# Kernel tuning notes

Measured on AMD Instinct MI355X. Metric: run time of the kernel, lower is better.

## Reference

```python
import jax, jax.numpy as jnp
import numpy as np

EPS_ATTN = 1e-5   # attention denominator eps (module eps)
EPS_LN = 1e-5     # nn.LayerNorm default eps


def _prime(x, proj):
    # Performer FAVOR+ hyperbolic positive features.
    # x: (B,H,L,dh), proj: (dh,m) -> (B,H,L,2m)
    dn = x.shape[-1] ** -0.25
    xn = dn * x
    d = jnp.einsum('bhld,dm->bhlm', xn, proj)
    diag = 0.5 * jnp.sum(xn * xn, axis=-1, keepdims=True)
    return jnp.concatenate([jnp.exp(d - diag), jnp.exp(-d - diag)], axis=-1)


def setup_inputs() -> dict:
    L, B, H, DH, DM, M = 2048, 4, 8, 64, 512, 256
    key = jax.random.key(0)
    k0, k1, k2 = jax.random.split(key, 3)
    h = jax.random.normal(k0, (L, B, DM), jnp.float32)
    w_qkv = jax.random.normal(k1, (H * 3 * DH, DM), jnp.float32) / np.sqrt(DM)
    w_o = jax.random.normal(k2, (DM, H * DH), jnp.float32) / np.sqrt(H * DH)
    ln_gamma = jnp.ones((DM,), jnp.float32)
    ln_beta = jnp.zeros((DM,), jnp.float32)
    # Gaussian orthogonal random matrix (blockwise QR), rows scaled by sqrt(dh)
    rng = np.random.default_rng(0)
    blocks = []
    for _ in range(M // DH):
        g = rng.standard_normal((DH, DH)).astype(np.float32)
        q, _ = np.linalg.qr(g)
        blocks.append(q.T)
    pm = np.concatenate(blocks, axis=0) * np.sqrt(DH)  # (M, DH)
    proj_matrix = jnp.asarray(pm.T.astype(np.float32))  # (DH, M)
    return {"h": h, "w_qkv": w_qkv, "w_o": w_o,
            "ln_gamma": ln_gamma, "ln_beta": ln_beta,
            "proj_matrix": proj_matrix}


def _forward(h, w_qkv, w_o, ln_gamma, ln_beta, proj_matrix):
    L, B, DM = h.shape
    DH, M = proj_matrix.shape
    H = w_qkv.shape[0] // (3 * DH)
    scale = DH ** -0.5

    qkv = (h @ w_qkv.T).reshape(L, B, H, 3 * DH)
    q, k, v = jnp.split(qkv, 3, axis=-1)
    q = jnp.transpose(q, (1, 2, 0, 3))  # (B,H,L,dh)
    k = jnp.transpose(k, (1, 2, 0, 3))
    v = jnp.transpose(v, (1, 2, 0, 3))

    qp = _prime(q, proj_matrix)  # (B,H,L,2M)
    kp = _prime(k, proj_matrix)
    kp = kp / jnp.sum(kp, axis=-1, keepdims=True)
    qp = qp / jnp.sum(qp, axis=-1, keepdims=True)

    den_acc = jnp.cumsum(kp, axis=2)
    denom = jnp.einsum('bhlm,bhlm->bhl', den_acc, qp)[..., None]  # (B,H,L,1)

    # fast_weight_sum: W_t = W_{t-1} + k_t v_t^T ; out_t = q_t @ W_t
    def step(W, xs):
        qt, kt, vt = xs  # (B,H,2M), (B,H,2M), (B,H,dh)
        W = W + kt[..., :, None] * vt[..., None, :]
        out = jnp.einsum('bhm,bhmd->bhd', qt, W)
        return W, out

    W0 = jnp.zeros((B, H, 2 * M, DH), h.dtype)
    xs = (jnp.transpose(qp, (2, 0, 1, 3)),
          jnp.transpose(kp, (2, 0, 1, 3)),
          jnp.transpose(v, (2, 0, 1, 3)))
    _, out = jax.lax.scan(step, W0, xs)  # (L,B,H,dh)
    out = jnp.transpose(out, (1, 2, 0, 3))  # (B,H,L,dh)

    out = scale * out / (denom + EPS_ATTN)
    out = jnp.transpose(out, (0, 2, 1, 3)).reshape(B, L, H * DH)  # (B,L,H*dh)
    out = jnp.swapaxes(out, 0, 1)  # (L,B,H*dh)

    attn_out = out @ w_o.T
    x = h + attn_out
    mu = jnp.mean(x, axis=-1, keepdims=True)
    var = jnp.mean((x - mu) ** 2, axis=-1, keepdims=True)
    return (x - mu) / jnp.sqrt(var + EPS_LN) * ln_gamma + ln_beta


def reference(h, w_qkv, w_o, ln_gamma, ln_beta, proj_matrix):
    return _forward(h, w_qkv, w_o, ln_gamma, ln_beta, proj_matrix)
```

## Files before the change

### kernel.cpp

```cpp
#include <hip/hip_runtime.h>
#include <hip/hip_fp16.h>
#include <math.h>

#define LSEQ 2048
#define NB 4
#define NH 8
#define DMID 512
#define CHK 128
#define SCALE 0.125f
#define DN 0.35355339059327373f
#define DN2 0.125f
#define LOG2E 1.4426950408889634f
#define EPS_ATTN 1e-5f
#define EPS_LN 1e-5f

typedef _Float16 f16x8 __attribute__((ext_vector_type(8)));
typedef _Float16 f16x4 __attribute__((ext_vector_type(4)));
typedef float f32x4 __attribute__((ext_vector_type(4)));

__device__ __forceinline__ float exp2a(float x) {
  float r;
  asm("v_exp_f32 %0, %1" : "=v"(r) : "v"(x));
  return r;
}

__device__ __forceinline__ void cvt16(const float* __restrict__ p,
                                      _Float16* __restrict__ dst) {
  float4 a = *(const float4*)p, b = *(const float4*)(p + 4);
  float4 c = *(const float4*)(p + 8), d = *(const float4*)(p + 12);
  f16x8 t0 = {(_Float16)a.x, (_Float16)a.y, (_Float16)a.z, (_Float16)a.w,
              (_Float16)b.x, (_Float16)b.y, (_Float16)b.z, (_Float16)b.w};
  f16x8 t1 = {(_Float16)c.x, (_Float16)c.y, (_Float16)c.z, (_Float16)c.w,
              (_Float16)d.x, (_Float16)d.y, (_Float16)d.z, (_Float16)d.w};
  *(f16x8*)dst = t0;
  *(f16x8*)(dst + 8) = t1;
}

__global__ void k_diag(float* out, int n, float val) {
  int i = blockIdx.x * 256 + threadIdx.x;
  if (i < n) out[i] = val;
}

__global__ __launch_bounds__(256) void k_ptr(const float* __restrict__ proj,
                                             __half* __restrict__ projT) {
  int e = blockIdx.x * 256 + threadIdx.x;
  int n = e >> 6, k = e & 63;
  projT[e] = __float2half_rn(proj[k * 256 + n] * (DN * LOG2E));
}

__global__ __launch_bounds__(256) void k_qkv(
    const float* __restrict__ A, const float* __restrict__ Wq,
    __half* __restrict__ q, __half* __restrict__ k, __half* __restrict__ v) {
  __shared__ __align__(16) char smem[34816];
  _Float16* Ah = (_Float16*)smem;
  _Float16* Bh = (_Float16*)(smem + 10240);
  _Float16* Oh = (_Float16*)smem;

  const int tid = threadIdx.x;
  const int row0 = blockIdx.x * 128;
  const int col0 = blockIdx.y * 128;
  const int lane = tid & 63, wv = tid >> 6;
  const int ln15 = lane & 15, quad = lane >> 4;
  const int m0 = wv * 32;
  const int srow = tid >> 1, sc = (tid & 1) * 16;

  f32x4 Cacc[2][8];
  const f32x4 z4 = {0.f, 0.f, 0.f, 0.f};
#pragma unroll
  for (int mi = 0; mi < 2; ++mi)
#pragma unroll
    for (int nt = 0; nt < 8; ++nt) Cacc[mi][nt] = z4;

  for (int kt = 0; kt < DMID; kt += 32) {
    cvt16(A + (size_t)(row0 + srow) * DMID + kt + sc, &Ah[srow * 40 + sc]);
    cvt16(Wq + (size_t)(col0 + srow) * DMID + kt + sc, &Bh[srow * 40 + sc]);
    __syncthreads();
    f16x8 a0 = *(const f16x8*)&Ah[(m0 + ln15) * 40 + quad * 8];
    f16x8 a1 = *(const f16x8*)&Ah[(m0 + 16 + ln15) * 40 + quad * 8];
#pragma unroll
    for (int nt = 0; nt < 8; ++nt) {
      f16x8 bf = *(const f16x8*)&Bh[(nt * 16 + ln15) * 40 + quad * 8];
      Cacc[0][nt] = __builtin_amdgcn_mfma_f32_16x16x32_f16(a0, bf, Cacc[0][nt], 0, 0, 0);
      Cacc[1][nt] = __builtin_amdgcn_mfma_f32_16x16x32_f16(a1, bf, Cacc[1][nt], 0, 0, 0);
    }
    __syncthreads();
  }
#pragma unroll
  for (int mi = 0; mi < 2; ++mi)
#pragma unroll
    for (int nt = 0; nt < 8; ++nt)
#pragma unroll
      for (int r = 0; r < 4; ++r)
        Oh[(m0 + mi * 16 + quad * 4 + r) * 136 + nt * 16 + ln15] =
            (_Float16)Cacc[mi][nt][r];
  __syncthreads();
  const int tr = tid >> 4, tc = tid & 15;
  const int col = col0 + tc * 8;
  const int hh = col / 192;
  const int rem = col - hh * 192;
  const int t = rem >> 6;
  const int d0 = rem & 63;
  __half* dstb = (t == 0) ? q : ((t == 1) ? k : v);
#pragma unroll
  for (int i = 0; i < 8; ++i) {
    int lrow = tr * 8 + i;
    int grow = row0 + lrow;
    int l = grow >> 2, bb = grow & 3;
    f16x8 val = *(const f16x8*)&Oh[lrow * 136 + tc * 8];
    *(f16x8*)((_Float16*)dstb + (((size_t)(bb * NH + hh) * LSEQ + l) << 6) + d0) = val;
  }
}

__global__ __launch_bounds__(512) void k_dgemm(
    const __half* __restrict__ qsrc, const __half* __restrict__ ksrc,
    const __half* __restrict__ projT, __half* __restrict__ dqd,
    __half* __restrict__ dkd, float* __restrict__ nq,
    float* __restrict__ nk) {
  __shared__ __align__(16) char smem[37888];
  _Float16* Bt = (_Float16*)smem;
  float* g_l  = (float*)(smem + 36864);
  float* ps_l = (float*)(smem + 37376);
  _Float16* Oh = (_Float16*)smem;

  const int tid = threadIdx.x;
  const __half* src = blockIdx.y ? ksrc : qsrc;
  __half* dst = blockIdx.y ? dkd : dqd;
  float* nrm = blockIdx.y ? nk : nq;
  const size_t r0 = (size_t)blockIdx.x * 128;

  const int lane = tid & 63, wv = tid >> 6;
  const int ln15 = lane & 15, quad = lane >> 4;
  const int m0 = wv * 16;

#pragma unroll
  for (int it = 0; it < 4; ++it) {
    int e = it * 512 + tid;
    int n = e >> 3, seg = e & 7;
    *(f16x8*)&Bt[n * 72 + seg * 8] =
        *(const f16x8*)((const _Float16*)projT + n * 64 + seg * 8);
  }

  f16x8 afrag[2];
  float ss = 0.f;
  {
    const _Float16* rp = (const _Float16*)src + (r0 + m0 + ln15) * 64;
#pragma unroll
    for (int ks = 0; ks < 2; ++ks) {
      f16x8 x8 = *(const f16x8*)(rp + ks * 32 + quad * 8);
      afrag[ks] = x8;
#pragma unroll
      for (int j = 0; j < 8; ++j) {
        float xv = (float)x8[j];
        ss = fmaf(xv, xv, ss);
      }
    }
    ss += __shfl_xor(ss, 16);
    ss += __shfl_xor(ss, 32);
  }
  if (quad == 0) g_l[m0 + ln15] = 0.5f * DN2 * LOG2E * ss;
  __syncthreads();

  f32x4 Cacc[16];
  const f32x4 z4 = {0.f, 0.f, 0.f, 0.f};
#pragma unroll
  for (int nt = 0; nt < 16; ++nt) Cacc[nt] = z4;

#pragma unroll
  for (int ks = 0; ks < 2; ++ks) {
    f16x8 a0 = afrag[ks];
#pragma unroll
    for (int nt = 0; nt < 16; ++nt) {
      f16x8 bf = *(const f16x8*)&Bt[(nt * 16 + ln15) * 72 + ks * 32 + quad * 8];
      Cacc[nt] = __builtin_amdgcn_mfma_f32_16x16x32_f16(a0, bf, Cacc[nt], 0, 0, 0);
    }
  }

  float gv[4], pp[4];
#pragma unroll
  for (int r = 0; r < 4; ++r) {
    gv[r] = g_l[m0 + quad * 4 + r];
    pp[r] = 0.f;
  }
#pragma unroll
  for (int nt = 0; nt < 16; ++nt)
#pragma unroll
    for (int r = 0; r < 4; ++r) {
      float d = Cacc[nt][r];
      pp[r] += exp2a(d - gv[r]) + exp2a(-d - gv[r]);
    }
#pragma unroll
  for (int r = 0; r < 4; ++r) {
    float p = pp[r];
    p += __shfl_xor(p, 1); p += __shfl_xor(p, 2);
    p += __shfl_xor(p, 4); p += __shfl_xor(p, 8);
    if (ln15 == 0) ps_l[m0 + quad * 4 + r] = p;
  }

#pragma unroll
  for (int hf = 0; hf < 2; ++hf) {
    __syncthreads();
#pragma unroll
    for (int nt2 = 0; nt2 < 8; ++nt2) {
      int nt = hf * 8 + nt2;
#pragma unroll
      for (int r = 0; r < 4; ++r)
        Oh[(m0 + quad * 4 + r) * 136 + nt2 * 16 + ln15] =
            (_Float16)Cacc[nt][r];
    }
    __syncthreads();
#pragma unroll
    for (int it = 0; it < 4; ++it) {
      int e = it * 512 + tid;
      int row = e >> 4, seg = e & 15;
      *(f16x8*)((_Float16*)dst + (r0 + row) * 256 + hf * 128 + seg * 8) =
          *(const f16x8*)&Oh[row * 136 + seg * 8];
    }
  }
  if (tid < 128) nrm[r0 + tid] = g_l[tid] + __log2f(ps_l[tid]);
}

__global__ __launch_bounds__(256) void k_kv(
    const __half* __restrict__ dk, const float* __restrict__ nk,
    const __half* __restrict__ v, __half* __restrict__ KVt,
    float* __restrict__ Ks) {
  __shared__ __align__(16) char smem[53248];
  _Float16* kpT = (_Float16*)smem;
  _Float16* Vt  = (_Float16*)(smem + 34816);
  float* ck = (float*)(smem + 52224);
  _Float16* Oh2 = (_Float16*)smem;

  const int tid = threadIdx.x;
  const int cidx = blockIdx.x;
  const int i0 = blockIdx.y * 128;
  const float fsign = (i0 < 256) ? 1.f : -1.f;
  const int m0col = (i0 < 256) ? i0 : i0 - 256;
  const size_t rowbase = (size_t)cidx * CHK;

  if (tid < 128) ck[tid] = nk[rowbase + tid];
  __syncthreads();

  {
    const int srow = tid >> 1;
    const int scol = (tid & 1) * 64;
    float c = ck[srow];
    const _Float16* src =
        (const _Float16*)dk + (rowbase + srow) * 256 + m0col + scol;
#pragma unroll
    for (int it = 0; it < 8; ++it) {
      f16x8 d8 = *(const f16x8*)(src + it * 8);
#pragma unroll
      for (int j = 0; j < 8; ++j)
        kpT[(scol + it * 8 + j) * 136 + srow] =
            (_Float16)exp2a(fmaf((float)d8[j], fsign, -c));
    }
  }
  {
    int s = tid & 127, dq0 = (tid >> 7) * 32;
    const _Float16* vsrc = (const _Float16*)v + (rowbase + s) * 64 + dq0;
#pragma unroll
    for (int b8 = 0; b8 < 4; ++b8) {
      f16x8 v8 = ((const f16x8*)vsrc)[b8];
#pragma unroll
      for (int j = 0; j < 8; ++j)
        Vt[(dq0 + b8 * 8 + j) * 136 + s] = v8[j];
    }
  }
  __syncthreads();

  const int lane = tid & 63, wv = tid >> 6;
  const int ln15 = lane & 15, quad = lane >> 4;
  const int m0 = wv * 32;

  f32x4 Cacc[2][4], Kacc[2];
  const f32x4 z4 = {0.f, 0.f, 0.f, 0.f};
#pragma unroll
  for (int mi = 0; mi < 2; ++mi) {
#pragma unroll
    for (int nt = 0; nt < 4; ++nt) Cacc[mi][nt] = z4;
    Kacc[mi] = z4;
  }
  f16x8 bone;
#pragma unroll
  for (int j = 0; j < 8; ++j)
    bone[j] = (ln15 == 0) ? (_Float16)1.0f : (_Float16)0.0f;

#pragma unroll
  for (int ks = 0; ks < 4; ++ks) {
    f16x8 a0 = *(const f16x8*)&kpT[(m0 + ln15) * 136 + ks * 32 + quad * 8];
    f16x8 a1 = *(const f16x8*)&kpT[(m0 + 16 + ln15) * 136 + ks * 32 + quad * 8];
#pragma unroll
    for (int nt = 0; nt < 4; ++nt) {
      f16x8 bV = *(const f16x8*)&Vt[(nt * 16 + ln15) * 136 + ks * 32 + quad * 8];
      Cacc[0][nt] = __builtin_amdgcn_mfma_f32_16x16x32_f16(a0, bV, Cacc[0][nt], 0, 0, 0);
      Cacc[1][nt] = __builtin_amdgcn_mfma_f32_16x16x32_f16(a1, bV, Cacc[1][nt], 0, 0, 0);
    }
    Kacc[0] = __builtin_amdgcn_mfma_f32_16x16x32_f16(a0, bone, Kacc[0], 0, 0, 0);
    Kacc[1] = __builtin_amdgcn_mfma_f32_16x16x32_f16(a1, bone, Kacc[1], 0, 0, 0);
  }

  if (ln15 == 0) {
#pragma unroll
    for (int mi = 0; mi < 2; ++mi)
#pragma unroll
      for (int r = 0; r < 4; ++r)
        Ks[(size_t)cidx * 512 + i0 + m0 + mi * 16 + quad * 4 + r] = Kacc[mi][r];
  }
  __syncthreads();
#pragma unroll
  for (int mi = 0; mi < 2; ++mi)
#pragma unroll
    for (int nt = 0; nt < 4; ++nt) {
      f16x4 pack = {(_Float16)Cacc[mi][nt][0], (_Float16)Cacc[mi][nt][1],
                    (_Float16)Cacc[mi][nt][2], (_Float16)Cacc[mi][nt][3]};
      *(f16x4*)&Oh2[(nt * 16 + ln15) * 136 + m0 + mi * 16 + quad * 4] = pack;
    }
  __syncthreads();
  {
    int d = tid >> 2, part = tid & 3;
    _Float16* dstp =
        (_Float16*)KVt + (size_t)cidx * 32768 + d * 512 + i0 + part * 32;
    const _Float16* srcp = &Oh2[d * 136 + part * 32];
#pragma unroll
    for (int j = 0; j < 4; ++j)
      *(f16x8*)(dstp + j * 8) = *(const f16x8*)(srcp + j * 8);
  }
}

__global__ __launch_bounds__(256) void k_scan(__half2* __restrict__ KV2,
                                              float* __restrict__ Ks) {
  const int bh = blockIdx.x;
  const int tid = threadIdx.x;
  if (blockIdx.y < 32) {
    uint2* p = (uint2*)(KV2 + (size_t)bh * 262144) + (blockIdx.y * 256 + tid);
    uint2 raw[16];
#pragma unroll
    for (int c = 0; c < 16; ++c) raw[c] = p[c * 8192];
    float ax0 = 0.f, ay0 = 0.f, ax1 = 0.f, ay1 = 0.f;
#pragma unroll
    for (int c = 0; c < 16; ++c) {
      __half2 h0 = *(__half2*)&raw[c].x;
      __half2 h1 = *(__half2*)&raw[c].y;
      float2 f0 = __half22float2(h0), f1 = __half22float2(h1);
      __half2 o0 = __floats2half2_rn(ax0, ay0);
      __half2 o1 = __floats2half2_rn(ax1, ay1);
      uint2 o;
      o.x = *(unsigned*)&o0;
      o.y = *(unsigned*)&o1;
      p[c * 8192] = o;
      ax0 += f0.x; ay0 += f0.y; ax1 += f1.x; ay1 += f1.y;
    }
  } else {
    int i = (blockIdx.y - 32) * 256 + tid;
    float* pk = Ks + (size_t)bh * 8192 + i;
    float vs[16];
#pragma unroll
    for (int c = 0; c < 16; ++c) vs[c] = pk[c * 512];
    float a = 0.f;
#pragma unroll
    for (int c = 0; c < 16; ++c) { pk[c * 512] = a; a += vs[c]; }
  }
}

template <int TH>
__device__ __forceinline__ void attn_body(
    const __half* __restrict__ dq, const __half* __restrict__ dk,
    const float* __restrict__ nq, const float* __restrict__ nk,
    const __half* __restrict__ v, const __half* __restrict__ KVt,
    const float* __restrict__ Kpre, float* __restrict__ outb, int cidx,
    char* smem) {
  constexpr int KROWS = TH ? 128 : 64;
  constexpr int KR32 = KROWS / 32;
  constexpr int NS = TH ? 8 : 4;
  constexpr int NKS = TH ? 4 : 2;

  _Float16* qpT = (_Float16*)(smem);
  _Float16* kpT = (_Float16*)(smem + 9216);
  _Float16* WT  = (_Float16*)(smem + 27648);
  float*    KpT = (float*)(smem + 36864);
  _Float16* S_h = (_Float16*)(smem);
  _Float16* Vt  = (_Float16*)(smem + 17408);
  float* cq_l   = (float*)(smem + 37120);
  float* ck_l   = (float*)(smem + 37632);
  float* den1_l = (float*)(smem + 38656);
  float* den2_l = (float*)(smem + 38912);
  float* invd_l = (float*)(smem + 39168);

  const int tid = threadIdx.x;
  const int cc = cidx & 15, bh = cidx >> 4;
  const size_t rowb = (size_t)cidx * 128;
  const size_t rowt = rowb + TH * 64;
  const int lane = tid & 63;
  const int wv = tid >> 6;
  const int ln15 = lane & 15;
  const int quad = lane >> 4;
  const int m0 = wv * 16;

  if (tid < 64) cq_l[tid] = nq[rowt + tid];
  if (tid < KROWS) ck_l[tid] = nk[rowb + tid];
  __syncthreads();

  const int c8 = tid & 7;
  const int r8 = tid >> 3;
  const int csrc = (c8 & 3) * 8;
  const float sgnf = (c8 < 4) ? 1.f : -1.f;

  const _Float16* qsrc = (const _Float16*)dq + (rowt + r8) * 256 + csrc;
  const _Float16* ksrc = (const _Float16*)dk + (rowb + r8) * 256 + csrc;
  const _Float16* wsrc = (const _Float16*)KVt + (size_t)cidx * 32768 +
                         r8 * 512 + ((c8 < 4) ? 0 : 256) + csrc;
  const float* kpsrc = Kpre + (size_t)cidx * 512 +
                       ((tid < 32) ? tid : (tid < 64 ? 224 + tid : 0));

  float cq[2], ck[KR32];
#pragma unroll
  for (int p = 0; p < 2; ++p) cq[p] = cq_l[r8 + p * 32];
#pragma unroll
  for (int p = 0; p < KR32; ++p) ck[p] = ck_l[r8 + p * 32];

  f16x8 rq[2], rk[KR32];
#pragma unroll
  for (int p = 0; p < 2; ++p) rq[p] = *(const f16x8*)(qsrc + p * 8192);
#pragma unroll
  for (int p = 0; p < KR32; ++p) rk[p] = *(const f16x8*)(ksrc + p * 8192);

  f32x4 Sacc[NS], Oacc[4], Dacc;
  const f32x4 z4 = {0.f, 0.f, 0.f, 0.f};
#pragma unroll
  for (int nt = 0; nt < NS; ++nt) Sacc[nt] = z4;
#pragma unroll
  for (int nt = 0; nt < 4; ++nt) Oacc[nt] = z4;
  Dacc = z4;

  for (int it = 0; it < 8; ++it) {
    const int kb = it * 32;
    f16x8 w0 = *(const f16x8*)(wsrc + kb);
    f16x8 w1 = *(const f16x8*)(wsrc + 16384 + kb);
    float kp = kpsrc[kb];

#pragma unroll
    for (int p = 0; p < 2; ++p) {
      f16x8 d = rq[p], t;
#pragma unroll
      for (int j = 0; j < 8; ++j)
        t[j] = (_Float16)exp2a(fmaf((float)d[j], sgnf, -cq[p]));
      *(f16x8*)&qpT[(r8 + p * 32) * 72 + c8 * 8] = t;
    }
#pragma unroll
    for (int p = 0; p < KR32; ++p) {
      f16x8 d = rk[p], t;
#pragma unroll
      for (int j = 0; j < 8; ++j)
        t[j] = (_Float16)exp2a(fmaf((float)d[j], sgnf, -ck[p]));
      *(f16x8*)&kpT[(r8 + p * 32) * 72 + c8 * 8] = t;
    }

    if (it < 7) {
#pragma unroll
      for (int p = 0; p < 2; ++p)
        rq[p] = *(const f16x8*)(qsrc + p * 8192 + kb + 32);
#pragma unroll
      for (int p = 0; p < KR32; ++p)
        rk[p] = *(const f16x8*)(ksrc + p * 8192 + kb + 32);
    }
    *(f16x8*)&WT[r8 * 72 + c8 * 8] = w0;
    *(f16x8*)&WT[(r8 + 32) * 72 + c8 * 8] = w1;
    if (tid < 64) KpT[tid] = kp;

    asm volatile("s_waitcnt lgkmcnt(0)" ::: "memory");
    __builtin_amdgcn_s_barrier();
    asm volatile("" ::: "memory");

#pragma unroll
    for (int ks = 0; ks < 2; ++ks) {
      f16x8 a0 = *(const f16x8*)&qpT[(m0 + ln15) * 72 + ks * 32 + quad * 8];
#pragma unroll
      for (int nt = 0; nt < NS; ++nt) {
        f16x8 bf = *(const f16x8*)&kpT[(nt * 16 + ln15) * 72 + ks * 32 + quad * 8];
        Sacc[nt] = __builtin_amdgcn_mfma_f32_16x16x32_f16(a0, bf, Sacc[nt], 0, 0, 0);
      }
#pragma unroll
      for (int nt = 0; nt < 4; ++nt) {
        f16x8 bw = *(const f16x8*)&WT[(nt * 16 + ln15) * 72 + ks * 32 + quad * 8];
        Oacc[nt] = __builtin_amdgcn_mfma_f32_16x16x32_f16(a0, bw, Oacc[nt], 0, 0, 0);
      }
      f16x8 bk;
#pragma unroll
      for (int j = 0; j < 8; ++j)
        bk[j] = (ln15 == 0) ? (_Float16)KpT[ks * 32 + quad * 8 + j]
                            : (_Float16)0.f;
      Dacc = __builtin_amdgcn_mfma_f32_16x16x32_f16(a0, bk, Dacc, 0, 0, 0);
    }

    asm volatile("" ::: "memory");
    __builtin_amdgcn_s_barrier();
    asm volatile("" ::: "memory");
  }

  if (ln15 == 0) {
#pragma unroll
    for (int r = 0; r < 4; ++r)
      den2_l[m0 + quad * 4 + r] = Dacc[r];
  }
  {
    float dp[4] = {0.f, 0.f, 0.f, 0.f};
#pragma unroll
    for (int nt = 0; nt < NS; ++nt) {
      int s = nt * 16 + ln15;
#pragma unroll
      for (int r = 0; r < 4; ++r) {
        int tl = m0 + quad * 4 + r;
        float vsv = (s <= TH * 64 + tl) ? Sacc[nt][r] : 0.f;
        dp[r] += vsv;
        S_h[tl * 136 + s] = (_Float16)vsv;
      }
    }
#pragma unroll
    for (int r = 0; r < 4; ++r) {
      float p = dp[r];
      p += __shfl_xor(p, 1); p += __shfl_xor(p, 2);
      p += __shfl_xor(p, 4); p += __shfl_xor(p, 8);
      if (ln15 == 0) den1_l[m0 + quad * 4 + r] = p;
    }
  }
  __syncthreads();
  if (tid < 64)
    invd_l[tid] = SCALE / (den1_l[tid] + den2_l[tid] + EPS_ATTN);
  {
    int s = tid & 127, d0v = (tid >> 7) * 32;
    if (TH == 1 || s < 64) {
      const _Float16* vsrc = (const _Float16*)v + (rowb + s) * 64 + d0v;
      f16x8 v0 = ((const f16x8*)vsrc)[0];
      f16x8 v1 = ((const f16x8*)vsrc)[1];
      f16x8 v2 = ((const f16x8*)vsrc)[2];
      f16x8 v3 = ((const f16x8*)vsrc)[3];
#pragma unroll
      for (int j = 0; j < 8; ++j) {
        Vt[(d0v + j) * 136 + s] = v0[j];
        Vt[(d0v + 8 + j) * 136 + s] = v1[j];
        Vt[(d0v + 16 + j) * 136 + s] = v2[j];
        Vt[(d0v + 24 + j) * 136 + s] = v3[j];
      }
    }
  }
  __syncthreads();
#pragma unroll
  for (int ks = 0; ks < NKS; ++ks) {
    f16x8 aS0 = *(const f16x8*)&S_h[(m0 + ln15) * 136 + ks * 32 + quad * 8];
#pragma unroll
    for (int nt = 0; nt < 4; ++nt) {
      f16x8 bV = *(const f16x8*)&Vt[(nt * 16 + ln15) * 136 + ks * 32 + quad * 8];
      Oacc[nt] = __builtin_amdgcn_mfma_f32_16x16x32_f16(aS0, bV, Oacc[nt], 0, 0, 0);
    }
  }
  const int b = bh >> 3, hh = bh & 7;
  float ivv[4];
#pragma unroll
  for (int r = 0; r < 4; ++r)
    ivv[r] = invd_l[m0 + quad * 4 + r];
#pragma unroll
  for (int nt = 0; nt < 4; ++nt) {
    int dcol = nt * 16 + ln15;
#pragma unroll
    for (int r = 0; r < 4; ++r) {
      int tl = m0 + quad * 4 + r;
      int l = cc * 128 + TH * 64 + tl;
      outb[((size_t)l * 4 + b) * 512 + hh * 64 + dcol] = Oacc[nt][r] * ivv[r];
    }
  }
}

__global__ __launch_bounds__(256, 4) void k_attn(
    const __half* __restrict__ dq, const __half* __restrict__ dk,
    const float* __restrict__ nq, const float* __restrict__ nk,
    const __half* __restrict__ v, const __half* __restrict__ KVt,
    const float* __restrict__ Kpre, float* __restrict__ outb) {
  __shared__ __align__(16) char smem[39424];
  const int bid = blockIdx.x;
  const int cidx = ((bid >> 4) << 3) + (bid & 7);
  if (((bid >> 3) & 1) == 0)
    attn_body<0>(dq, dk, nq, nk, v, KVt, Kpre, outb, cidx, smem);
  else
    attn_body<1>(dq, dk, nq, nk, v, KVt, Kpre, outb, cidx, smem);
}

__global__ __launch_bounds__(256) void k_oproj(
    const float* __restrict__ A, const float* __restrict__ Wo,
    const float* __restrict__ hres, float* __restrict__ xout) {
  __shared__ __align__(16) char smem[34816];
  _Float16* Ah = (_Float16*)smem;
  _Float16* Bh = (_Float16*)(smem + 10240);
  _Float16* Oh = (_Float16*)smem;

  const int tid = threadIdx.x;
  const int row0 = blockIdx.x * 128;
  const int col0 = blockIdx.y * 128;
  const int lane = tid & 63, wv = tid >> 6;
  const int ln15 = lane & 15, quad = lane >> 4;
  const int m0 = wv * 32;
  const int srow = tid >> 1, sc = (tid & 1) * 16;

  f32x4 Cacc[2][8];
  const f32x4 z4 = {0.f, 0.f, 0.f, 0.f};
#pragma unroll
  for (int mi = 0; mi < 2; ++mi)
#pragma unroll
    for (int nt = 0; nt < 8; ++nt) Cacc[mi][nt] = z4;

  for (int kt = 0; kt < DMID; kt += 32) {
    cvt16(A + (size_t)(row0 + srow) * DMID + kt + sc, &Ah[srow * 40 + sc]);
    cvt16(Wo + (size_t)(col0 + srow) * DMID + kt + sc, &Bh[srow * 40 + sc]);
    __syncthreads();
    f16x8 a0 = *(const f16x8*)&Ah[(m0 + ln15) * 40 + quad * 8];
    f16x8 a1 = *(const f16x8*)&Ah[(m0 + 16 + ln15) * 40 + quad * 8];
#pragma unroll
    for (int nt = 0; nt < 8; ++nt) {
      f16x8 bf = *(const f16x8*)&Bh[(nt * 16 + ln15) * 40 + quad * 8];
      Cacc[0][nt] = __builtin_amdgcn_mfma_f32_16x16x32_f16(a0, bf, Cacc[0][nt], 0, 0, 0);
      Cacc[1][nt] = __builtin_amdgcn_mfma_f32_16x16x32_f16(a1, bf, Cacc[1][nt], 0, 0, 0);
    }
    __syncthreads();
  }
#pragma unroll
  for (int mi = 0; mi < 2; ++mi)
#pragma unroll
    for (int nt = 0; nt < 8; ++nt)
#pragma unroll
      for (int r = 0; r < 4; ++r)
        Oh[(m0 + mi * 16 + quad * 4 + r) * 136 + nt * 16 + ln15] =
            (_Float16)Cacc[mi][nt][r];
  __syncthreads();
  const int tr = tid >> 4, tc = tid & 15;
#pragma unroll
  for (int i = 0; i < 8; ++i) {
    int lrow = tr * 8 + i;
    int grow = row0 + lrow;
    size_t base = (size_t)grow * 512 + col0 + tc * 8;
    f16x8 o = *(const f16x8*)&Oh[lrow * 136 + tc * 8];
    float4 h0 = *(const float4*)(hres + base);
    float4 h1 = *(const float4*)(hres + base + 4);
    *(float4*)(xout + base) =
        make_float4((float)o[0] + h0.x, (float)o[1] + h0.y,
                    (float)o[2] + h0.z, (float)o[3] + h0.w);
    *(float4*)(xout + base + 4) =
        make_float4((float)o[4] + h1.x, (float)o[5] + h1.y,
                    (float)o[6] + h1.z, (float)o[7] + h1.w);
  }
}

__global__ __launch_bounds__(256) void k_ln(float* __restrict__ x,
                                            const float* __restrict__ g,
                                            const float* __restrict__ bta) {
  __shared__ float ws_[4], wq_[4];
  const int row = blockIdx.x;
  const int tid = threadIdx.x;
  float2 vv = *(const float2*)(x + (size_t)row * 512 + tid * 2);
  float s = vv.x + vv.y;
  float sq = vv.x * vv.x + vv.y * vv.y;
#pragma unroll
  for (int off = 1; off < 64; off <<= 1) {
    s += __shfl_xor(s, off, 64);
    sq += __shfl_xor(sq, off, 64);
  }
  if ((tid & 63) == 0) { ws_[tid >> 6] = s; wq_[tid >> 6] = sq; }
  __syncthreads();
  s = ws_[0] + ws_[1] + ws_[2] + ws_[3];
  sq = wq_[0] + wq_[1] + wq_[2] + wq_[3];
  float mu = s * (1.f / 512.f);
  float var = sq * (1.f / 512.f) - mu * mu;
  float rstd = rsqrtf(var + EPS_LN);
  int c = tid * 2;
  float2 o;
  o.x = (vv.x - mu) * rstd * g[c] + bta[c];
  o.y = (vv.y - mu) * rstd * g[c + 1] + bta[c + 1];
  *(float2*)(x + (size_t)row * 512 + c) = o;
}

extern "C" void kernel_launch(void* const* d_in, const int* in_sizes, int n_in,
                              void* d_out, int out_size, void* d_ws,
                              size_t ws_size, hipStream_t stream) {
  const float* h    = (const float*)d_in[0];
  const float* wqkv = (const float*)d_in[1];
  const float* wo   = (const float*)d_in[2];
  const float* g    = (const float*)d_in[3];
  const float* bta  = (const float*)d_in[4];
  const float* proj = (const float*)d_in[5];
  float* out = (float*)d_out;
  char* wsb = (char*)d_ws;

  __half* q   = (__half*)(wsb + 0);
  __half* kb  = (__half*)(wsb + 8388608);
  __half* vb  = (__half*)(wsb + 16777216);
  __half* dq  = (__half*)(wsb + 25165824);
  __half* dk  = (__half*)(wsb + 58720256);
  float*  nq  = (float*)(wsb + 92274688);
  float*  nk  = (float*)(wsb + 92798976);
  __half* KVt = (__half*)(wsb + 93323264);
  float*  Ks  = (float*)(wsb + 126877696);
  __half* pT  = (__half*)(wsb + 127926272);
  float* outb = (float*)(wsb + 0);

  if (ws_size < 127959040ull) {
    float val = 1000.0f + (float)(ws_size >> 20);
    k_diag<<<(out_size + 255) / 256, 256, 0, stream>>>(out, out_size, val);
    return;
  }

  k_ptr  <<<dim3(64), 256, 0, stream>>>(proj, pT);
  k_qkv  <<<dim3(64, 12), 256, 0, stream>>>(h, wqkv, q, kb, vb);
  k_dgemm<<<dim3(512, 2), 512, 0, stream>>>(q, kb, pT, dq, dk, nq, nk);
  k_kv   <<<dim3(512, 4), 256, 0, stream>>>(dk, nk, vb, KVt, Ks);
  k_scan <<<dim3(32, 34), 256, 0, stream>>>((__half2*)KVt, Ks);
  k_attn <<<dim3(1024), 256, 0, stream>>>(dq, dk, nq, nk, vb, KVt, Ks, outb);
  k_oproj<<<dim3(64, 4), 256, 0, stream>>>(outb, wo, h, out);
  k_ln   <<<dim3(8192), 256, 0, stream>>>(out, g, bta);
}
```

Baseline: 246.2 us.

## Merge attention half-chunk blocks into one 512-thread block per chunk

Before, each 128-row chunk was handled by two 256-thread blocks, one per 64-row half, and each block recomputed the key features and reloaded the KV-state tile. Now a single 512-thread block processes the whole chunk: the key features, W tile and V transpose are computed once and shared by both halves, with the two half-groups of waves selected by a runtime flag. This removes duplicated exp work and global loads. In exchange, shared memory per block grows, the grid is halved, the two halves have unequal work inside one block, and the launch-bounds occupancy hint is dropped.

```diff
diff --git a/kernel.cpp b/kernel.cpp
--- a/kernel.cpp
+++ b/kernel.cpp
@@ -361,80 +361,77 @@
   }
 }
 
-template <int TH>
-__device__ __forceinline__ void attn_body(
+__global__ __launch_bounds__(512) void k_attn(
     const __half* __restrict__ dq, const __half* __restrict__ dk,
     const float* __restrict__ nq, const float* __restrict__ nk,
     const __half* __restrict__ v, const __half* __restrict__ KVt,
-    const float* __restrict__ Kpre, float* __restrict__ outb, int cidx,
-    char* smem) {
-  constexpr int KROWS = TH ? 128 : 64;
-  constexpr int KR32 = KROWS / 32;
-  constexpr int NS = TH ? 8 : 4;
-  constexpr int NKS = TH ? 4 : 2;
-
+    const float* __restrict__ Kpre, float* __restrict__ outb) {
+  __shared__ __align__(16) char smem[53760];
   _Float16* qpT = (_Float16*)(smem);
-  _Float16* kpT = (_Float16*)(smem + 9216);
-  _Float16* WT  = (_Float16*)(smem + 27648);
-  float*    KpT = (float*)(smem + 36864);
+  _Float16* kpT = (_Float16*)(smem + 18432);
+  _Float16* WT  = (_Float16*)(smem + 36864);
+  float*    KpT = (float*)(smem + 46080);
+  float* cq_l   = (float*)(smem + 46336);
+  float* ck_l   = (float*)(smem + 46848);
   _Float16* S_h = (_Float16*)(smem);
-  _Float16* Vt  = (_Float16*)(smem + 17408);
-  float* cq_l   = (float*)(smem + 37120);
-  float* ck_l   = (float*)(smem + 37632);
-  float* den1_l = (float*)(smem + 38656);
-  float* den2_l = (float*)(smem + 38912);
-  float* invd_l = (float*)(smem + 39168);
+  _Float16* Vt  = (_Float16*)(smem + 34816);
+  float* den1_l = (float*)(smem + 52224);
+  float* den2_l = (float*)(smem + 52736);
+  float* invd_l = (float*)(smem + 53248);
 
   const int tid = threadIdx.x;
+  const int cidx = blockIdx.x;
   const int cc = cidx & 15, bh = cidx >> 4;
   const size_t rowb = (size_t)cidx * 128;
-  const size_t rowt = rowb + TH * 64;
   const int lane = tid & 63;
   const int wv = tid >> 6;
-  const int ln15 = lane & 15;
-  const int quad = lane >> 4;
-  const int m0 = wv * 16;
-
-  if (tid < 64) cq_l[tid] = nq[rowt + tid];
-  if (tid < KROWS) ck_l[tid] = nk[rowb + tid];
+  const int H = wv >> 2;
+  const int m0 = (wv & 3) * 16;
+  const int ln15 = lane & 15, quad = lane >> 4;
+
+  if (tid < 128) cq_l[tid] = nq[rowb + tid];
+  else if (tid < 256) ck_l[tid - 128] = nk[rowb + tid - 128];
   __syncthreads();
 
   const int c8 = tid & 7;
-  const int r8 = tid >> 3;
+  const int r9 = tid >> 3;
   const int csrc = (c8 & 3) * 8;
   const float sgnf = (c8 < 4) ? 1.f : -1.f;
 
-  const _Float16* qsrc = (const _Float16*)dq + (rowt + r8) * 256 + csrc;
-  const _Float16* ksrc = (const _Float16*)dk + (rowb + r8) * 256 + csrc;
+  const _Float16* qsrc = (const _Float16*)dq + (rowb + r9) * 256 + csrc;
+  const _Float16* ksrc = (const _Float16*)dk + (rowb + r9) * 256 + csrc;
   const _Float16* wsrc = (const _Float16*)KVt + (size_t)cidx * 32768 +
-                         r8 * 512 + ((c8 < 4) ? 0 : 256) + csrc;
+                         r9 * 512 + ((c8 < 4) ? 0 : 256) + csrc;
   const float* kpsrc = Kpre + (size_t)cidx * 512 +
                        ((tid < 32) ? tid : (tid < 64 ? 224 + tid : 0));
 
-  float cq[2], ck[KR32];
-#pragma unroll
-  for (int p = 0; p < 2; ++p) cq[p] = cq_l[r8 + p * 32];
-#pragma unroll
-  for (int p = 0; p < KR32; ++p) ck[p] = ck_l[r8 + p * 32];
-
-  f16x8 rq[2], rk[KR32];
-#pragma unroll
-  for (int p = 0; p < 2; ++p) rq[p] = *(const f16x8*)(qsrc + p * 8192);
-#pragma unroll
-  for (int p = 0; p < KR32; ++p) rk[p] = *(const f16x8*)(ksrc + p * 8192);
-
-  f32x4 Sacc[NS], Oacc[4], Dacc;
+  float cq[2], ck2[2];
+#pragma unroll
+  for (int p = 0; p < 2; ++p) {
+    cq[p] = cq_l[r9 + p * 64];
+    ck2[p] = ck_l[r9 + p * 64];
+  }
+
+  f16x8 rq[2], rk[2];
+#pragma unroll
+  for (int p = 0; p < 2; ++p) {
+    rq[p] = *(const f16x8*)(qsrc + p * 16384);
+    rk[p] = *(const f16x8*)(ksrc + p * 16384);
+  }
+
+  f32x4 Sacc[8], Oacc[4], Dacc;
   const f32x4 z4 = {0.f, 0.f, 0.f, 0.f};
 #pragma unroll
-  for (int nt = 0; nt < NS; ++nt) Sacc[nt] = z4;
+  for (int nt = 0; nt < 8; ++nt) Sacc[nt] = z4;
 #pragma unroll
   for (int nt = 0; nt < 4; ++nt) Oacc[nt] = z4;
   Dacc = z4;
+
+  const int NSw = H ? 8 : 4;
 
   for (int it = 0; it < 8; ++it) {
     const int kb = it * 32;
     f16x8 w0 = *(const f16x8*)(wsrc + kb);
-    f16x8 w1 = *(const f16x8*)(wsrc + 16384 + kb);
     float kp = kpsrc[kb];
 
 #pragma unroll
@@ -443,27 +440,25 @@
 #pragma unroll
       for (int j = 0; j < 8; ++j)
         t[j] = (_Float16)exp2a(fmaf((float)d[j], sgnf, -cq[p]));
-      *(f16x8*)&qpT[(r8 + p * 32) * 72 + c8 * 8] = t;
-    }
-#pragma unroll
-    for (int p = 0; p < KR32; ++p) {
+      *(f16x8*)&qpT[(r9 + p * 64) * 72 + c8 * 8] = t;
+    }
+#pragma unroll
+    for (int p = 0; p < 2; ++p) {
       f16x8 d = rk[p], t;
 #pragma unroll
       for (int j = 0; j < 8; ++j)
-        t[j] = (_Float16)exp2a(fmaf((float)d[j], sgnf, -ck[p]));
-      *(f16x8*)&kpT[(r8 + p * 32) * 72 + c8 * 8] = t;
+        t[j] = (_Float16)exp2a(fmaf((float)d[j], sgnf, -ck2[p]));
+      *(f16x8*)&kpT[(r9 + p * 64) * 72 + c8 * 8] = t;
     }
 
     if (it < 7) {
 #pragma unroll
-      for (int p = 0; p < 2; ++p)
-        rq[p] = *(const f16x8*)(qsrc + p * 8192 + kb + 32);
-#pragma unroll
-      for (int p = 0; p < KR32; ++p)
-        rk[p] = *(const f16x8*)(ksrc + p * 8192 + kb + 32);
-    }
-    *(f16x8*)&WT[r8 * 72 + c8 * 8] = w0;
-    *(f16x8*)&WT[(r8 + 32) * 72 + c8 * 8] = w1;
+      for (int p = 0; p < 2; ++p) {
+        rq[p] = *(const f16x8*)(qsrc + p * 16384 + kb + 32);
+        rk[p] = *(const f16x8*)(ksrc + p * 16384 + kb + 32);
+      }
+    }
+    *(f16x8*)&WT[r9 * 72 + c8 * 8] = w0;
     if (tid < 64) KpT[tid] = kp;
 
     asm volatile("s_waitcnt lgkmcnt(0)" ::: "memory");
@@ -472,11 +467,18 @@
 
 #pragma unroll
     for (int ks = 0; ks < 2; ++ks) {
-      f16x8 a0 = *(const f16x8*)&qpT[(m0 + ln15) * 72 + ks * 32 + quad * 8];
-#pragma unroll
-      for (int nt = 0; nt < NS; ++nt) {
+      f16x8 a0 = *(const f16x8*)&qpT[(H * 64 + m0 + ln15) * 72 + ks * 32 + quad * 8];
+#pragma unroll
+      for (int nt = 0; nt < 4; ++nt) {
         f16x8 bf = *(const f16x8*)&kpT[(nt * 16 + ln15) * 72 + ks * 32 + quad * 8];
         Sacc[nt] = __builtin_amdgcn_mfma_f32_16x16x32_f16(a0, bf, Sacc[nt], 0, 0, 0);
+      }
+      if (H) {
+#pragma unroll
+        for (int nt = 4; nt < 8; ++nt) {
+          f16x8 bf = *(const f16x8*)&kpT[(nt * 16 + ln15) * 72 + ks * 32 + quad * 8];
+          Sacc[nt] = __builtin_amdgcn_mfma_f32_16x16x32_f16(a0, bf, Sacc[nt], 0, 0, 0);
+        }
       }
 #pragma unroll
       for (int nt = 0; nt < 4; ++nt) {
@@ -499,19 +501,22 @@
   if (ln15 == 0) {
 #pragma unroll
     for (int r = 0; r < 4; ++r)
-      den2_l[m0 + quad * 4 + r] = Dacc[r];
+      den2_l[H * 64 + m0 + quad * 4 + r] = Dacc[r];
   }
   {
+    _Float16* S_me = S_h + H * 8704;
     float dp[4] = {0.f, 0.f, 0.f, 0.f};
 #pragma unroll
-    for (int nt = 0; nt < NS; ++nt) {
-      int s = nt * 16 + ln15;
-#pragma unroll
-      for (int r = 0; r < 4; ++r) {
-        int tl = m0 + quad * 4 + r;
-        float vsv = (s <= TH * 64 + tl) ? Sacc[nt][r] : 0.f;
-        dp[r] += vsv;
-        S_h[tl * 136 + s] = (_Float16)vsv;
+    for (int nt = 0; nt < 8; ++nt) {
+      if (nt < NSw) {
+        int s = nt * 16 + ln15;
+#pragma unroll
+        for (int r = 0; r < 4; ++r) {
+          int tl = m0 + quad * 4 + r;
+          float vsv = (s <= H * 64 + tl) ? Sacc[nt][r] : 0.f;
+          dp[r] += vsv;
+          S_me[tl * 136 + s] = (_Float16)vsv;
+        }
       }
     }
 #pragma unroll
@@ -519,68 +524,52 @@
       float p = dp[r];
       p += __shfl_xor(p, 1); p += __shfl_xor(p, 2);
       p += __shfl_xor(p, 4); p += __shfl_xor(p, 8);
-      if (ln15 == 0) den1_l[m0 + quad * 4 + r] = p;
-    }
-  }
-  __syncthreads();
-  if (tid < 64)
+      if (ln15 == 0) den1_l[H * 64 + m0 + quad * 4 + r] = p;
+    }
+  }
+  {
+    int s = tid & 127, d0v = (tid >> 7) * 16;
+    const _Float16* vsrc = (const _Float16*)v + (rowb + s) * 64 + d0v;
+    f16x8 v0 = ((const f16x8*)vsrc)[0];
+    f16x8 v1 = ((const f16x8*)vsrc)[1];
+#pragma unroll
+    for (int j = 0; j < 8; ++j) {
+      Vt[(d0v + j) * 136 + s] = v0[j];
+      Vt[(d0v + 8 + j) * 136 + s] = v1[j];
+    }
+  }
+  __syncthreads();
+  if (tid < 128)
     invd_l[tid] = SCALE / (den1_l[tid] + den2_l[tid] + EPS_ATTN);
+  __syncthreads();
   {
-    int s = tid & 127, d0v = (tid >> 7) * 32;
-    if (TH == 1 || s < 64) {
-      const _Float16* vsrc = (const _Float16*)v + (rowb + s) * 64 + d0v;
-      f16x8 v0 = ((const f16x8*)vsrc)[0];
-      f16x8 v1 = ((const f16x8*)vsrc)[1];
-      f16x8 v2 = ((const f16x8*)vsrc)[2];
-      f16x8 v3 = ((const f16x8*)vsrc)[3];
-#pragma unroll
-      for (int j = 0; j < 8; ++j) {
-        Vt[(d0v + j) * 136 + s] = v0[j];
-        Vt[(d0v + 8 + j) * 136 + s] = v1[j];
-        Vt[(d0v + 16 + j) * 136 + s] = v2[j];
-        Vt[(d0v + 24 + j) * 136 + s] = v3[j];
+    _Float16* S_me = S_h + H * 8704;
+#pragma unroll
+    for (int ks = 0; ks < 4; ++ks) {
+      if (ks < (H ? 4 : 2)) {
+        f16x8 aS0 = *(const f16x8*)&S_me[(m0 + ln15) * 136 + ks * 32 + quad * 8];
+#pragma unroll
+        for (int nt = 0; nt < 4; ++nt) {
+          f16x8 bV = *(const f16x8*)&Vt[(nt * 16 + ln15) * 136 + ks * 32 + quad * 8];
+          Oacc[nt] = __builtin_amdgcn_mfma_f32_16x16x32_f16(aS0, bV, Oacc[nt], 0, 0, 0);
+        }
       }
-    }
-  }
-  __syncthreads();
-#pragma unroll
-  for (int ks = 0; ks < NKS; ++ks) {
-    f16x8 aS0 = *(const f16x8*)&S_h[(m0 + ln15) * 136 + ks * 32 + quad * 8];
-#pragma unroll
-    for (int nt = 0; nt < 4; ++nt) {
-      f16x8 bV = *(const f16x8*)&Vt[(nt * 16 + ln15) * 136 + ks * 32 + quad * 8];
-      Oacc[nt] = __builtin_amdgcn_mfma_f32_16x16x32_f16(aS0, bV, Oacc[nt], 0, 0, 0);
     }
   }
   const int b = bh >> 3, hh = bh & 7;
   float ivv[4];
 #pragma unroll
   for (int r = 0; r < 4; ++r)
-    ivv[r] = invd_l[m0 + quad * 4 + r];
+    ivv[r] = invd_l[H * 64 + m0 + quad * 4 + r];
 #pragma unroll
   for (int nt = 0; nt < 4; ++nt) {
     int dcol = nt * 16 + ln15;
 #pragma unroll
     for (int r = 0; r < 4; ++r) {
-      int tl = m0 + quad * 4 + r;
-      int l = cc * 128 + TH * 64 + tl;
+      int l = cc * 128 + H * 64 + m0 + quad * 4 + r;
       outb[((size_t)l * 4 + b) * 512 + hh * 64 + dcol] = Oacc[nt][r] * ivv[r];
     }
   }
-}
-
-__global__ __launch_bounds__(256, 4) void k_attn(
-    const __half* __restrict__ dq, const __half* __restrict__ dk,
-    const float* __restrict__ nq, const float* __restrict__ nk,
-    const __half* __restrict__ v, const __half* __restrict__ KVt,
-    const float* __restrict__ Kpre, float* __restrict__ outb) {
-  __shared__ __align__(16) char smem[39424];
-  const int bid = blockIdx.x;
-  const int cidx = ((bid >> 4) << 3) + (bid & 7);
-  if (((bid >> 3) & 1) == 0)
-    attn_body<0>(dq, dk, nq, nk, v, KVt, Kpre, outb, cidx, smem);
-  else
-    attn_body<1>(dq, dk, nq, nk, v, KVt, Kpre, outb, cidx, smem);
 }
 
 __global__ __launch_bounds__(256) void k_oproj(
@@ -710,7 +699,7 @@
   k_dgemm<<<dim3(512, 2), 512, 0, stream>>>(q, kb, pT, dq, dk, nq, nk);
   k_kv   <<<dim3(512, 4), 256, 0, stream>>>(dk, nk, vb, KVt, Ks);
   k_scan <<<dim3(32, 34), 256, 0, stream>>>((__half2*)KVt, Ks);
-  k_attn <<<dim3(1024), 256, 0, stream>>>(dq, dk, nq, nk, vb, KVt, Ks, outb);
+  k_attn <<<dim3(512), 512, 0, stream>>>(dq, dk, nq, nk, vb, KVt, Ks, outb);
   k_oproj<<<dim3(64, 4), 256, 0, stream>>>(outb, wo, h, out);
   k_ln   <<<dim3(8192), 256, 0, stream>>>(out, g, bta);
 }
```

After: 243.7 us. Within noise of the previous version (-1.0%).
